# Kernel tuning notes

Measured on AMD Instinct MI355X. Metric: run time of the kernel, lower is better.

The kernel has to match this reference:

```python
import jax, jax.numpy as jnp
import numpy as np

NUM_ROUTING = 3

def squash(v, axis=-1):
    # scale = s2 / (1 + s2) / sqrt(s2), same as the TF source (no epsilon)
    s2 = jnp.sum(jnp.square(v), axis=axis, keepdims=True)
    scale = s2 / (1.0 + s2) / jnp.sqrt(s2)
    return scale * v


def setup_inputs() -> dict:
    key = jax.random.key(0)
    k1, k2 = jax.random.split(key)
    B, I, D = 128, 1152, 8   # batch, input_num_capsule, input_dim_vector
    C, E = 32, 16            # num_capsule, dim_vector
    x = jax.random.normal(k1, (B, I, D), dtype=jnp.float32)
    W = jax.random.normal(k2, (I, C, D, E), dtype=jnp.float32) * 0.05
    return {"x": x, "W": W}


def reference(x, W):
    # x: [B, I, D]; W: [I, C, D, E]
    B, I, D = x.shape
    C, E = W.shape[1], W.shape[3]
    # inputs_hat: u_hat[b,i,c,e] = sum_d x[b,i,d] * W[i,c,d,e]
    # (the TF code serializes this over batch via tf.scan; math is a batched GEMM)
    u_hat = jnp.einsum('bid,icde->bice', x, W)  # [B, I, C, E]
    # routing logits; TF bias has shape [1, I, C, 1, 1] and becomes per-batch
    # [B, I, C, 1, 1] after the first += (broadcast). We track [*, I, C].
    b = jnp.zeros((1, I, C), dtype=x.dtype)
    outputs = None
    for i in range(NUM_ROUTING):
        c = jax.nn.softmax(b, axis=2)[..., None]           # [*, I, C, 1]
        s = jnp.sum(c * u_hat, axis=1, keepdims=True)      # [B, 1, C, E]
        outputs = squash(s)                                # [B, 1, C, E]
        if i != NUM_ROUTING - 1:
            b = b + jnp.sum(u_hat * outputs, axis=-1)      # [B, I, C]
    return outputs.reshape(B, C, E)
```

## Files before the change

kernel.cpp:

```cpp
#include <hip/hip_runtime.h>
#include <hip/hip_fp16.h>
#include <math.h>

#define BATCH 128
#define NI    1152
#define ND    8
#define NC    32
#define NE    16
#define NROUT 3

#define ISPLIT     48
#define ICHUNK     (NI / ISPLIT)
#define BT         8
#define NB         2
#define RT_THREADS 256
#define SQ_THREADS 256
#define PREP_TPB   2

typedef _Float16 h2 __attribute__((ext_vector_type(2)));
typedef unsigned int uint;

__device__ __forceinline__ h2 cvt_pk(float a, float b) {
    auto r = __builtin_amdgcn_cvt_pkrtz(a, b);
    union { decltype(r) i; h2 o; } u; u.i = r; return u.o;
}
__device__ __forceinline__ uint h2u(h2 v) { union { h2 h; uint u; } x; x.h = v; return x.u; }
__device__ __forceinline__ h2 u2h(uint v) { union { uint u; h2 h; } x; x.u = v; return x.h; }

#if __has_builtin(__builtin_amdgcn_fdot2)
#define FDOT2(a, b, c) __builtin_amdgcn_fdot2((a), (b), (c), false)
#else
__device__ __forceinline__ float FDOT2(h2 a, h2 b, float c) {
    return c + (float)a.x * (float)b.x + (float)a.y * (float)b.y;
}
#endif

template<int CTRL>
__device__ __forceinline__ float dpp_add(float v) {
    int t = __builtin_amdgcn_update_dpp(0, __float_as_int(v), CTRL, 0xF, 0xF, true);
    return v + __int_as_float(t);
}

__device__ __forceinline__ float xor32_sum(float v) {
#if __has_builtin(__builtin_amdgcn_permlane32_swap)
    auto r = __builtin_amdgcn_permlane32_swap(__float_as_int(v), __float_as_int(v), false, false);
    return __int_as_float(r[0]) + __int_as_float(r[1]);
#else
    return v + __shfl_xor(v, 32);
#endif
}
__device__ __forceinline__ float xor16_sum(float v) {
#if __has_builtin(__builtin_amdgcn_permlane16_swap)
    auto r = __builtin_amdgcn_permlane16_swap(__float_as_int(v), __float_as_int(v), false, false);
    return __int_as_float(r[0]) + __int_as_float(r[1]);
#else
    int s = __builtin_amdgcn_ds_swizzle(__float_as_int(v), 0x401F);
    return v + __int_as_float(s);
#endif
}

__device__ __forceinline__ float sum_over_e8(float v) {
    v = dpp_add<0xB1>(v);
    v = dpp_add<0x4E>(v);
    v = dpp_add<0x141>(v);
    return v;
}

__global__ __launch_bounds__(RT_THREADS)
void prep_kernel(const float* __restrict__ W, uint4* __restrict__ W_h)
{
    __shared__ float ls[PREP_TPB][NC * 132];

    const int tid = threadIdx.x;
    const size_t i0 = (size_t)blockIdx.x * PREP_TPB;

    const float4* src = (const float4*)(W + i0 * (NC * ND * NE));
#pragma unroll
    for (int t = 0; t < PREP_TPB; ++t) {
#pragma unroll
        for (int r = 0; r < 4; ++r) {
            int g = tid + r * RT_THREADS;
            float4 v = src[t * 1024 + g];
            *(float4*)&ls[t][(g >> 5) * 132 + (g & 31) * 4] = v;
        }
    }
    __syncthreads();

#pragma unroll
    for (int t = 0; t < PREP_TPB; ++t) {
#pragma unroll
        for (int r = 0; r < 2; ++r) {
            int g  = tid + r * RT_THREADS;
            int er = g >> 6, ehh = (g >> 5) & 1, c = g & 31;
            int e  = ehh * 8 + er;
            const float* p = &ls[t][c * 132 + e];
            uint4 o;
            o.x = h2u(cvt_pk(p[0],  p[16]));
            o.y = h2u(cvt_pk(p[32], p[48]));
            o.z = h2u(cvt_pk(p[64], p[80]));
            o.w = h2u(cvt_pk(p[96], p[112]));
            W_h[(i0 + t) * 512 + g] = o;
        }
    }
}

__global__ __launch_bounds__(RT_THREADS)
void route_iter_kernel(const float* __restrict__ x, const uint4* __restrict__ W_h,
                       const float* __restrict__ o_sum, __half* __restrict__ s_part,
                       int iter)
{
    const int tid = threadIdx.x;
    const int c   = tid & 31;
    const int eh  = (tid >> 5) & 1;
    int wid;
    asm("v_mov_b32 %0, %1" : "=v"(wid) : "v"(tid >> 6));
    const int ic  = blockIdx.x;
    const int bt  = blockIdx.y;
    const int i0  = ic * ICHUNK;
    const int b0  = bt * BT + wid * NB;
    const int e0  = eh * 8;

    float o_reg[NB][8];
    if (iter > 0) {
#pragma unroll
        for (int j = 0; j < NB; ++j) {
            const float4* op = (const float4*)(o_sum + ((size_t)(b0 + j) * NC + c) * NE + e0);
            float4 a = op[0], b = op[1];
            o_reg[j][0] = a.x; o_reg[j][1] = a.y; o_reg[j][2] = a.z; o_reg[j][3] = a.w;
            o_reg[j][4] = b.x; o_reg[j][5] = b.y; o_reg[j][6] = b.z; o_reg[j][7] = b.w;
        }
    }

    float s_acc[NB][8];
#pragma unroll
    for (int j = 0; j < NB; ++j)
#pragma unroll
        for (int e = 0; e < 8; ++e) s_acc[j][e] = 0.f;

    const uint4* wp = W_h + (size_t)i0 * 512 + eh * 32 + c;

    const float* xp[NB];
    float4 xnA[NB][2], xnB[NB][2];
#pragma unroll
    for (int j = 0; j < NB; ++j) {
        xp[j] = x + ((size_t)(b0 + j) * NI + i0) * ND;
        xnA[j][0] = *(const float4*)xp[j];
        xnA[j][1] = *(const float4*)(xp[j] + 4);
    }
    uint4 wvA[8], wvB[8];
#pragma unroll
    for (int er = 0; er < 8; ++er) wvA[er] = wp[er * 64];
    wp += 512;

    auto body = [&](const float4 (&XC)[NB][2], float4 (&XN)[NB][2],
                    const uint4 (&WC)[8], uint4 (&WN)[8], int II) {
        if (II + 1 < ICHUNK) {
#pragma unroll
            for (int er = 0; er < 8; ++er) WN[er] = wp[er * 64];
            wp += 512;
#pragma unroll
            for (int j = 0; j < NB; ++j) {
                xp[j] += ND;
                XN[j][0] = *(const float4*)xp[j];
                XN[j][1] = *(const float4*)(xp[j] + 4);
            }
        }

        h2 xq[NB][4];
#pragma unroll
        for (int j = 0; j < NB; ++j) {
            xq[j][0] = cvt_pk(XC[j][0].x, XC[j][0].y);
            xq[j][1] = cvt_pk(XC[j][0].z, XC[j][0].w);
            xq[j][2] = cvt_pk(XC[j][1].x, XC[j][1].y);
            xq[j][3] = cvt_pk(XC[j][1].z, XC[j][1].w);
        }

        float uh[NB][8];
#pragma unroll
        for (int er = 0; er < 8; ++er) {
            h2 w0 = u2h(WC[er].x), w1 = u2h(WC[er].y);
            h2 w2 = u2h(WC[er].z), w3 = u2h(WC[er].w);
#pragma unroll
            for (int j = 0; j < NB; ++j) {
                float acc = 0.f;
                acc = FDOT2(xq[j][0], w0, acc);
                acc = FDOT2(xq[j][1], w1, acc);
                acc = FDOT2(xq[j][2], w2, acc);
                acc = FDOT2(xq[j][3], w3, acc);
                uh[j][er] = acc;
            }
        }

        if (iter > 0) {
#pragma unroll
            for (int j = 0; j < NB; ++j) {
                float lp = 0.f;
#pragma unroll
                for (int e = 0; e < 8; ++e) lp = fmaf(uh[j][e], o_reg[j][e], lp);
                lp = xor32_sum(lp);
                float el = __expf(lp);
                float v = dpp_add<0x140>(dpp_add<0x141>(
                          dpp_add<0x4E>(dpp_add<0xB1>(el))));
                float den = xor16_sum(v);
                float wgt = el * __builtin_amdgcn_rcpf(den);
#pragma unroll
                for (int e = 0; e < 8; ++e) s_acc[j][e] = fmaf(wgt, uh[j][e], s_acc[j][e]);
            }
        } else {
            const float wgt = 1.f / 32.f;
#pragma unroll
            for (int j = 0; j < NB; ++j)
#pragma unroll
                for (int e = 0; e < 8; ++e) s_acc[j][e] = fmaf(wgt, uh[j][e], s_acc[j][e]);
        }
    };

    for (int r2 = 0; r2 < ICHUNK / 2; ++r2) {
        body(xnA, xnB, wvA, wvB, 2 * r2);
        body(xnB, xnA, wvB, wvA, 2 * r2 + 1);
    }

#pragma unroll
    for (int j = 0; j < NB; ++j) {
        __half* base = s_part + (((size_t)ic * BATCH + (b0 + j)) * NC + c) * NE + e0;
        union { __half2 h2v[4]; uint4 u; } pk;
#pragma unroll
        for (int q = 0; q < 4; ++q)
            pk.h2v[q] = __floats2half2_rn(s_acc[j][2*q], s_acc[j][2*q+1]);
        *(uint4*)base = pk.u;
    }
}

__global__ __launch_bounds__(SQ_THREADS)
void squash_kernel(const __half* __restrict__ s_part, float* __restrict__ o_sum,
                   float* __restrict__ out, int iter)
{
    const int base2 = (blockIdx.x * SQ_THREADS + threadIdx.x) * 2;

    float a0 = 0.f, a1 = 0.f;
#pragma unroll 8
    for (int k = 0; k < ISPLIT; ++k) {
        __half2 v = *(const __half2*)(s_part + (size_t)k * (BATCH * NC * NE) + base2);
        a0 += __low2float(v);
        a1 += __high2float(v);
    }

    float q = sum_over_e8(a0 * a0 + a1 * a1);
    float scale = sqrtf(q) / (1.f + q);
    float o0 = scale * a0, o1 = scale * a1;

    if (iter == NROUT - 1) {
        *(float2*)(out + base2) = make_float2(o0, o1);
    } else if (iter == 0) {
        *(float2*)(o_sum + base2) = make_float2(o0, o1);
    } else {
        float2 prev = *(float2*)(o_sum + base2);
        *(float2*)(o_sum + base2) = make_float2(prev.x + o0, prev.y + o1);
    }
}

extern "C" void kernel_launch(void* const* d_in, const int* in_sizes, int n_in,
                              void* d_out, int out_size, void* d_ws, size_t ws_size,
                              hipStream_t stream) {
    const float* x = (const float*)d_in[0];
    const float* W = (const float*)d_in[1];
    float* out = (float*)d_out;

    uint4*  W_h    = (uint4*)d_ws;
    __half* s_part = (__half*)(W_h + (size_t)NI * 512);
    float*  o_sum  = (float*)(s_part + (size_t)ISPLIT * BATCH * NC * NE);

    prep_kernel<<<NI / PREP_TPB, RT_THREADS, 0, stream>>>(W, W_h);

    for (int it = 0; it < NROUT; ++it) {
        route_iter_kernel<<<dim3(ISPLIT, BATCH / BT), RT_THREADS, 0, stream>>>(
            x, W_h, o_sum, s_part, it);
        squash_kernel<<<(BATCH * NC * NE) / (SQ_THREADS * 2), SQ_THREADS, 0, stream>>>(
            s_part, o_sum, out, it);
    }
}
```

Before: 114.5 us.

## Stage fp16 W tiles through LDS with padded layout in routing kernel

The routing kernel now copies groups of 8 input-capsule W tiles from global memory into shared memory and has each thread read its weights from LDS, instead of every thread streaming its own register-double-buffered global loads. The prep kernel writes W in a padded per-capsule row layout (68 words per row) so the LDS reads avoid bank conflicts. This is meant to cut redundant global/L2 traffic and register pressure. In exchange it adds block-wide barriers per group and loses the overlap of W prefetch with compute.

```diff
diff --git a/kernel.cpp b/kernel.cpp
--- a/kernel.cpp
+++ b/kernel.cpp
@@ -11,9 +11,13 @@
 
 #define ISPLIT     48
 #define ICHUNK     (NI / ISPLIT)
+#define GTILES     8
+#define NGROUP     (ICHUNK / GTILES)
 #define BT         8
 #define NB         2
 #define RT_THREADS 256
+#define CROW       68
+#define TLDSW      (NC * CROW)
 #define SQ_THREADS 256
 #define PREP_TPB   2
 
@@ -67,7 +71,7 @@
 }
 
 __global__ __launch_bounds__(RT_THREADS)
-void prep_kernel(const float* __restrict__ W, uint4* __restrict__ W_h)
+void prep_kernel(const float* __restrict__ W, uint* __restrict__ W_hp)
 {
     __shared__ float ls[PREP_TPB][NC * 132];
 
@@ -90,25 +94,26 @@
     for (int t = 0; t < PREP_TPB; ++t) {
 #pragma unroll
         for (int r = 0; r < 2; ++r) {
-            int g  = tid + r * RT_THREADS;
-            int er = g >> 6, ehh = (g >> 5) & 1, c = g & 31;
-            int e  = ehh * 8 + er;
+            int g = tid + r * RT_THREADS;
+            int c = g >> 4, e = g & 15;
             const float* p = &ls[t][c * 132 + e];
             uint4 o;
             o.x = h2u(cvt_pk(p[0],  p[16]));
             o.y = h2u(cvt_pk(p[32], p[48]));
             o.z = h2u(cvt_pk(p[64], p[80]));
             o.w = h2u(cvt_pk(p[96], p[112]));
-            W_h[(i0 + t) * 512 + g] = o;
+            *(uint4*)&W_hp[(i0 + t) * TLDSW + c * CROW + e * 4] = o;
         }
     }
 }
 
 __global__ __launch_bounds__(RT_THREADS)
-void route_iter_kernel(const float* __restrict__ x, const uint4* __restrict__ W_h,
+void route_iter_kernel(const float* __restrict__ x, const uint* __restrict__ W_hp,
                        const float* __restrict__ o_sum, __half* __restrict__ s_part,
                        int iter)
 {
+    __shared__ uint Wh[GTILES * TLDSW];
+
     const int tid = threadIdx.x;
     const int c   = tid & 31;
     const int eh  = (tid >> 5) & 1;
@@ -137,8 +142,6 @@
 #pragma unroll
         for (int e = 0; e < 8; ++e) s_acc[j][e] = 0.f;
 
-    const uint4* wp = W_h + (size_t)i0 * 512 + eh * 32 + c;
-
     const float* xp[NB];
     float4 xnA[NB][2], xnB[NB][2];
 #pragma unroll
@@ -147,17 +150,11 @@
         xnA[j][0] = *(const float4*)xp[j];
         xnA[j][1] = *(const float4*)(xp[j] + 4);
     }
-    uint4 wvA[8], wvB[8];
-#pragma unroll
-    for (int er = 0; er < 8; ++er) wvA[er] = wp[er * 64];
-    wp += 512;
-
-    auto body = [&](const float4 (&XC)[NB][2], float4 (&XN)[NB][2],
-                    const uint4 (&WC)[8], uint4 (&WN)[8], int II) {
+
+    const uint* wbase = &Wh[c * CROW + e0 * 4];
+
+    auto body = [&](const float4 (&XC)[NB][2], float4 (&XN)[NB][2], int t, int II) {
         if (II + 1 < ICHUNK) {
-#pragma unroll
-            for (int er = 0; er < 8; ++er) WN[er] = wp[er * 64];
-            wp += 512;
 #pragma unroll
             for (int j = 0; j < NB; ++j) {
                 xp[j] += ND;
@@ -175,11 +172,12 @@
             xq[j][3] = cvt_pk(XC[j][1].z, XC[j][1].w);
         }
 
+        const uint* wr = wbase + t * TLDSW;
         float uh[NB][8];
 #pragma unroll
         for (int er = 0; er < 8; ++er) {
-            h2 w0 = u2h(WC[er].x), w1 = u2h(WC[er].y);
-            h2 w2 = u2h(WC[er].z), w3 = u2h(WC[er].w);
+            uint4 wv = *(const uint4*)(wr + er * 4);
+            h2 w0 = u2h(wv.x), w1 = u2h(wv.y), w2 = u2h(wv.z), w3 = u2h(wv.w);
 #pragma unroll
             for (int j = 0; j < NB; ++j) {
                 float acc = 0.f;
@@ -215,9 +213,22 @@
         }
     };
 
-    for (int r2 = 0; r2 < ICHUNK / 2; ++r2) {
-        body(xnA, xnB, wvA, wvB, 2 * r2);
-        body(xnB, xnA, wvB, wvA, 2 * r2 + 1);
+    for (int g = 0; g < NGROUP; ++g) {
+        if (g) __syncthreads();
+        {
+            const uint4* src = (const uint4*)(W_hp + (size_t)(i0 + g * GTILES) * TLDSW);
+            uint4* dst = (uint4*)Wh;
+#pragma unroll
+            for (int k = 0; k < (GTILES * TLDSW / 4) / RT_THREADS; ++k)
+                dst[tid + k * RT_THREADS] = src[tid + k * RT_THREADS];
+        }
+        __syncthreads();
+
+#pragma unroll
+        for (int tp = 0; tp < GTILES / 2; ++tp) {
+            body(xnA, xnB, 2 * tp,     g * GTILES + 2 * tp);
+            body(xnB, xnA, 2 * tp + 1, g * GTILES + 2 * tp + 1);
+        }
     }
 
 #pragma unroll
@@ -266,15 +277,15 @@
     const float* W = (const float*)d_in[1];
     float* out = (float*)d_out;
 
-    uint4*  W_h    = (uint4*)d_ws;
-    __half* s_part = (__half*)(W_h + (size_t)NI * 512);
+    uint*   W_hp   = (uint*)d_ws;
+    __half* s_part = (__half*)(W_hp + (size_t)NI * TLDSW);
     float*  o_sum  = (float*)(s_part + (size_t)ISPLIT * BATCH * NC * NE);
 
-    prep_kernel<<<NI / PREP_TPB, RT_THREADS, 0, stream>>>(W, W_h);
+    prep_kernel<<<NI / PREP_TPB, RT_THREADS, 0, stream>>>(W, W_hp);
 
     for (int it = 0; it < NROUT; ++it) {
         route_iter_kernel<<<dim3(ISPLIT, BATCH / BT), RT_THREADS, 0, stream>>>(
-            x, W_h, o_sum, s_part, it);
+            x, W_hp, o_sum, s_part, it);
         squash_kernel<<<(BATCH * NC * NE) / (SQ_THREADS * 2), SQ_THREADS, 0, stream>>>(
             s_part, o_sum, out, it);
     }
```

Result: faster. 112.0 us (-2.2%).
